# Kernel tuning notes

Hardware: AMD Instinct MI355X
Metric: run time of the kernel (lower is better)

## Reference

```python
import jax, jax.numpy as jnp
import numpy as np

DIM = 2048          # args.dim
E = 16              # n_routed_experts
TOPK = 2            # n_activated_experts
H = 1408            # moe_inter_dim (expert hidden)
N_SHARED = 2        # n_shared_experts
HS = H * N_SHARED   # shared expert hidden
B, S = 2, 2048
TEMP = 1.0          # gate_temperature


def setup_inputs() -> dict:
    key = jax.random.key(0)
    ks = jax.random.split(key, 8)
    sc = 0.02
    return {
        "x": jax.random.normal(ks[0], (B, S, DIM), dtype=jnp.float32),
        "gate_w": jax.random.normal(ks[1], (E, DIM), dtype=jnp.float32) * sc,
        "w1": jax.random.normal(ks[2], (E, H, DIM), dtype=jnp.float32) * sc,
        "w2": jax.random.normal(ks[3], (E, DIM, H), dtype=jnp.float32) * sc,
        "w3": jax.random.normal(ks[4], (E, H, DIM), dtype=jnp.float32) * sc,
        "sw1": jax.random.normal(ks[5], (HS, DIM), dtype=jnp.float32) * sc,
        "sw2": jax.random.normal(ks[6], (DIM, HS), dtype=jnp.float32) * sc,
        "sw3": jax.random.normal(ks[7], (HS, DIM), dtype=jnp.float32) * sc,
    }


def reference(x, gate_w, w1, w2, w3, sw1, sw2, sw3):
    b, s, d = x.shape
    xf = x.reshape(-1, d)  # [T, D]

    # shared expert (SwiGLU FFN)
    sh = jax.nn.silu(xf @ sw1.T) * (xf @ sw3.T)      # [T, HS]
    shared_out = sh @ sw2.T                           # [T, D]

    # gate (eval mode: no input noise)
    scores = (xf @ gate_w.T) / TEMP                   # [T, E]
    probs = jax.nn.softmax(scores, axis=-1)
    topk_vals, topk_idx = jax.lax.top_k(probs, TOPK)  # sorted desc, matches torch.topk
    topk_vals = topk_vals / (topk_vals.sum(-1, keepdims=True) + 1e-9)

    # combine weights per (token, expert); zero where expert not selected
    w = (jax.nn.one_hot(topk_idx, E, dtype=xf.dtype) * topk_vals[..., None]).sum(1)  # [T, E]

    # all-expert SwiGLU, weighted-combined (w==0 exactly zeroes unselected experts)
    h1 = jnp.einsum('td,ehd->teh', xf, w1)            # [T, E, H]
    h3 = jnp.einsum('td,ehd->teh', xf, w3)
    act = jax.nn.silu(h1) * h3 * w[:, :, None]
    y = jnp.einsum('teh,edh->td', act, w2) + shared_out

    # aux load-balancing loss
    importance = probs.mean(0)                        # [E]
    load = w.sum(0) / (w.sum() + 1e-9)                # [E]
    aux_loss = E * (importance * load).sum()

    return y.reshape(b, s, d), aux_loss
```

## Files before the change

### kernel.cpp

```cpp
#include <hip/hip_runtime.h>
#include <cstdint>

#define TOKS 4096
#define DIMD 2048
#define NE   16
#define HE   1408
#define HSH  2816
#define SLOTS 8192
#define SLOTP 8320
#define MAXT 2048

typedef unsigned short u16;
typedef __attribute__((ext_vector_type(8))) __bf16 bf16x8;
typedef __attribute__((ext_vector_type(4))) float  f32x4;

__device__ inline unsigned f2bf_pack(float a, float b) {
  unsigned ua = __builtin_bit_cast(unsigned, a);
  unsigned ub = __builtin_bit_cast(unsigned, b);
  ua = (ua + 0x7FFFu + ((ua >> 16) & 1u)) >> 16;
  ub = (ub + 0x7FFFu + ((ub >> 16) & 1u)) >> 16;
  return ua | (ub << 16);
}
__device__ inline u16 f2bf(float a) {
  unsigned ua = __builtin_bit_cast(unsigned, a);
  return (u16)((ua + 0x7FFFu + ((ua >> 16) & 1u)) >> 16);
}
__device__ inline float bf2f(u16 u) {
  return __builtin_bit_cast(float, (unsigned)u << 16);
}
__device__ inline void gload_lds16(const u16* g, u16* l) {
  __builtin_amdgcn_global_load_lds((const __attribute__((address_space(1))) void*)g,
                                   (__attribute__((address_space(3))) void*)l, 16, 0, 0);
}

__global__ __launch_bounds__(64)
void gate2_kernel(const float* __restrict__ x, const float* __restrict__ gw,
                  float* __restrict__ probs, int* __restrict__ sel0, int* __restrict__ sel1,
                  float* __restrict__ wt0, float* __restrict__ wt1,
                  u16* __restrict__ xbf)
{
  const int t = blockIdx.x;
  const int l = threadIdx.x;
  const float4* xr = (const float4*)(x + (size_t)t * DIMD);
  float4 xv[8];
#pragma unroll
  for (int j = 0; j < 8; ++j) xv[j] = xr[j * 64 + l];

  uint2* xo = (uint2*)(xbf + (size_t)t * DIMD);
#pragma unroll
  for (int j = 0; j < 8; ++j) {
    uint2 q; q.x = f2bf_pack(xv[j].x, xv[j].y); q.y = f2bf_pack(xv[j].z, xv[j].w);
    xo[j * 64 + l] = q;
  }

  float sc[16];
#pragma unroll
  for (int e = 0; e < 16; ++e) {
    const float4* g = (const float4*)(gw + (size_t)e * DIMD);
    float s = 0.f;
#pragma unroll
    for (int j = 0; j < 8; ++j) {
      float4 gv = g[j * 64 + l];
      s += xv[j].x * gv.x + xv[j].y * gv.y + xv[j].z * gv.z + xv[j].w * gv.w;
    }
#pragma unroll
    for (int o = 32; o > 0; o >>= 1) s += __shfl_down(s, o);
    sc[e] = s;
  }
  if (l == 0) {
    float mx = sc[0];
#pragma unroll
    for (int e = 1; e < 16; ++e) mx = fmaxf(mx, sc[e]);
    float pe[16]; float sum = 0.f;
#pragma unroll
    for (int e = 0; e < 16; ++e) { pe[e] = __expf(sc[e] - mx); sum += pe[e]; }
    float inv = 1.f / sum;
    int b0 = -1, b1 = -1; float v0 = -1.f, v1 = -1.f;
#pragma unroll
    for (int e = 0; e < 16; ++e) {
      float p = pe[e] * inv;
      probs[t * 16 + e] = p;
      if (p > v0) { v1 = v0; b1 = b0; v0 = p; b0 = e; }
      else if (p > v1) { v1 = p; b1 = e; }
    }
    float wsum = v0 + v1 + 1e-9f;
    sel0[t] = b0; sel1[t] = b1;
    wt0[t] = v0 / wsum; wt1[t] = v1 / wsum;
  }
}

__global__ __launch_bounds__(256)
void expert_count(const int* __restrict__ sel0, const int* __restrict__ sel1,
                  const float* __restrict__ wt0, const float* __restrict__ wt1,
                  int* __restrict__ counts, float* __restrict__ loadsum)
{
  const int e = blockIdx.x, tid = threadIdx.x;
  int c = 0; float s = 0.f;
  for (int t = tid; t < TOKS; t += 256) {
    if (sel0[t] == e) { c++; s += wt0[t]; }
    else if (sel1[t] == e) { c++; s += wt1[t]; }
  }
  __shared__ int ci[256]; __shared__ float sf[256];
  ci[tid] = c; sf[tid] = s; __syncthreads();
  for (int d = 128; d > 0; d >>= 1) {
    if (tid < d) { ci[tid] += ci[tid + d]; sf[tid] += sf[tid + d]; }
    __syncthreads();
  }
  if (tid == 0) { counts[e] = ci[0]; loadsum[e] = sf[0]; }
}

__global__ __launch_bounds__(256)
void offsets_aux(const float* __restrict__ probs, const int* __restrict__ counts,
                 const float* __restrict__ loadsum, int* __restrict__ offs,
                 int* __restrict__ te2, int* __restrict__ tn2, int* __restrict__ tm2,
                 int* __restrict__ me2,
                 int* __restrict__ te3, int* __restrict__ tn3, int* __restrict__ tm3,
                 int* __restrict__ me3,
                 float* __restrict__ out_aux)
{
  const int tid = threadIdx.x;
  float imp[16];
#pragma unroll
  for (int e = 0; e < 16; ++e) imp[e] = 0.f;
  for (int t = tid; t < TOKS; t += 256)
#pragma unroll
    for (int e = 0; e < 16; ++e) imp[e] += probs[t * 16 + e];

  __shared__ float red[256];
  __shared__ float impE[16];
  for (int e = 0; e < 16; ++e) {
    red[tid] = imp[e]; __syncthreads();
    for (int d = 128; d > 0; d >>= 1) {
      if (tid < d) red[tid] += red[tid + d];
      __syncthreads();
    }
    if (tid == 0) impE[e] = red[0];
    __syncthreads();
  }
  if (tid == 0) {
    int off = 0;
    for (int e = 0; e < 16; ++e) { offs[e] = off; off += counts[e]; }
    float tot = 0.f;
    for (int e = 0; e < 16; ++e) tot += loadsum[e];
    float aux = 0.f;
    for (int e = 0; e < 16; ++e) aux += (impE[e] / (float)TOKS) * (loadsum[e] / (tot + 1e-9f));
    *out_aux = 16.f * aux;
  }
  __syncthreads();
  if (tid < 16) {
    int e = tid;
    int mt_e = (counts[e] + 127) >> 7;
    {
      int base = 0;
      for (int ee = 0; ee < e; ++ee) base += ((counts[ee] + 127) >> 7) * 22;
      int idx = base;
      for (int n = 0; n < 22; ++n)
        for (int m = 0; m < mt_e; ++m) { te2[idx] = e; tn2[idx] = n; tm2[idx] = m << 7; ++idx; }
      if (e == 15) me2[0] = idx;
    }
    {
      int base = 0;
      for (int ee = 0; ee < e; ++ee) base += ((counts[ee] + 127) >> 7) * 16;
      int idx = base;
      for (int n = 0; n < 16; ++n)
        for (int m = 0; m < mt_e; ++m) { te3[idx] = e; tn3[idx] = n; tm3[idx] = m << 7; ++idx; }
      if (e == 15) me3[0] = idx;
    }
  }
}

__global__ __launch_bounds__(256)
void rank_scatter(const int* __restrict__ sel0, const int* __restrict__ sel1,
                  const float* __restrict__ wt0, const float* __restrict__ wt1,
                  const int* __restrict__ offs, int* __restrict__ toklist2,
                  float* __restrict__ slotwt, int* __restrict__ tokslot)
{
  const int e = blockIdx.x, tid = threadIdx.x;
  const int t0 = tid * 16;
  unsigned flags = 0; int cloc = 0;
#pragma unroll
  for (int j = 0; j < 16; ++j) {
    int t = t0 + j;
    bool f = (sel0[t] == e) || (sel1[t] == e);
    flags |= ((unsigned)f) << j;
    cloc += f;
  }
  __shared__ int psum[256];
  psum[tid] = cloc; __syncthreads();
  for (int d = 1; d < 256; d <<= 1) {
    int v = (tid >= d) ? psum[tid - d] : 0;
    __syncthreads();
    psum[tid] += v;
    __syncthreads();
  }
  int r = offs[e] + psum[tid] - cloc;
  for (int j = 0; j < 16; ++j) {
    if ((flags >> j) & 1u) {
      int t = t0 + j;
      bool first = (sel0[t] == e);
      toklist2[r] = t;
      slotwt[r] = first ? wt0[t] : wt1[t];
      tokslot[2 * t + (first ? 0 : 1)] = r;
      r++;
    }
  }
}

__global__ __launch_bounds__(256)
void cvt_f32_bf16(const float4* __restrict__ src, uint2* __restrict__ dst, int n4)
{
  int i = blockIdx.x * 256 + threadIdx.x;
  int stride = gridDim.x * 256;
  for (; i < n4; i += stride) {
    float4 v = src[i];
    uint2 p; p.x = f2bf_pack(v.x, v.y); p.y = f2bf_pack(v.z, v.w);
    dst[i] = p;
  }
}

__global__ __launch_bounds__(256)
void cvt_pair(const float4* __restrict__ src1, const float4* __restrict__ src3,
              uint2* __restrict__ dst, int rows, int k4, int dstride4, int total4)
{
  int i = blockIdx.x * 256 + threadIdx.x;
  int stride = gridDim.x * 256;
  int per_e = rows * k4;
  for (; i < total4; i += stride) {
    int e = i / per_e;
    int rem = i - e * per_e;
    int j = rem / k4;
    int c = rem - j * k4;
    size_t dbase = (size_t)e * dstride4 + (size_t)(((j >> 6) * 128 + (j & 63))) * k4 + c;
    float4 v1 = src1[i];
    uint2 p1; p1.x = f2bf_pack(v1.x, v1.y); p1.y = f2bf_pack(v1.z, v1.w);
    dst[dbase] = p1;
    float4 v3 = src3[i];
    uint2 p3; p3.x = f2bf_pack(v3.x, v3.y); p3.y = f2bf_pack(v3.z, v3.w);
    dst[dbase + (size_t)64 * k4] = p3;
  }
}

__global__ __launch_bounds__(256)
void gather2(const u16* __restrict__ xbf, const int* __restrict__ toklist2,
             u16* __restrict__ Xg)
{
  int slot = blockIdx.x * 4 + (threadIdx.x >> 6);
  int l = threadIdx.x & 63;
  int tok = toklist2[slot];
  const uint2* srcr = (const uint2*)(xbf + (size_t)tok * DIMD);
  uint2* dstr = (uint2*)(Xg + (size_t)slot * DIMD);
#pragma unroll
  for (int j = 0; j < 8; ++j) dstr[j * 64 + l] = srcr[j * 64 + l];
}

template<int MODE>
__global__ __launch_bounds__(256, 4)
void gemm128(const u16* __restrict__ A, const u16* __restrict__ Bg,
             u16* __restrict__ Obf, float* __restrict__ Of,
             const int* __restrict__ counts, const int* __restrict__ offs,
             const int* __restrict__ te, const int* __restrict__ tn,
             const int* __restrict__ tm, const int* __restrict__ meta,
             const float* __restrict__ slotwt)
{
  constexpr int KD = (MODE == 0) ? DIMD : (MODE == 1) ? HSH : (MODE == 2) ? DIMD : HE;
  constexpr int ND = (MODE == 0) ? 2 * HSH : (MODE == 1) ? DIMD : (MODE == 2) ? HSH : DIMD;
  constexpr bool FUSE = (MODE == 0 || MODE == 2);
  constexpr int NDOUT = (MODE == 0) ? HSH : (MODE == 2) ? HE : ND;

  __shared__ __align__(16) char sMemRaw[FUSE ? 36864 : 32768];
  u16* sA = (u16*)sMemRaw;
  u16* sB = sA + 128 * 64;

  const int tid  = threadIdx.x;
  const int lane = tid & 63;
  const int wave = tid >> 6;
  const int wm = wave >> 1, wn = wave & 1;

  int mbase, nbase;
  int e = 0, cnt = 0, arow0;
  const u16* B = Bg;
  if constexpr (MODE >= 2) {
    int tix = blockIdx.x;
    if (tix >= meta[0]) return;
    e = te[tix];
    cnt = counts[e];
    mbase = tm[tix];
    nbase = tn[tix] * 128;
    arow0 = offs[e] + mbase;
    B = Bg + (size_t)e * ND * KD;
  } else {
    const int nx = gridDim.x;
    int bid = blockIdx.y * nx + blockIdx.x;
    int cpx = (nx * gridDim.y) >> 3;
    int swz = (bid & 7) * cpx + (bid >> 3);
    mbase = (swz / nx) * 128;
    nbase = (swz % nx) * 128;
    arow0 = mbase;
  }

  f32x4 acc[4][4];
#pragma unroll
  for (int i = 0; i < 4; ++i)
#pragma unroll
    for (int j = 0; j < 4; ++j) acc[i][j] = (f32x4){0.f, 0.f, 0.f, 0.f};

  const int srow  = lane >> 3;
  const int sslot = (lane & 7) ^ srow;
  const int scol  = sslot * 8;

  const u16* Bbase = B + (size_t)nbase * KD;

  for (int kb = 0; kb < KD; kb += 64) {
#pragma unroll
    for (int i = 0; i < 4; ++i) {
      int c = wave * 4 + i;
      int row = c * 8 + srow;
      size_t ar;
      if constexpr (MODE >= 2) {
        int rg = arow0 + row;
        if (rg > SLOTS - 1) rg = SLOTS - 1;
        ar = (size_t)rg * KD;
      } else {
        ar = (size_t)(arow0 + row) * KD;
      }
      gload_lds16(A + ar + kb + scol, &sA[c * 512]);
      gload_lds16(Bbase + (size_t)row * KD + kb + scol, &sB[c * 512]);
    }
    __syncthreads();

#pragma unroll
    for (int ks = 0; ks < 2; ++ks) {
      bf16x8 a[4], b[4];
#pragma unroll
      for (int mi = 0; mi < 4; ++mi) {
        int r = wm * 64 + mi * 16 + (lane & 15);
        int s = (ks * 4 + (lane >> 4)) ^ (r & 7);
        a[mi] = *(const bf16x8*)((const char*)sA + r * 128 + s * 16);
      }
#pragma unroll
      for (int ni = 0; ni < 4; ++ni) {
        int r = wn * 64 + ni * 16 + (lane & 15);
        int s = (ks * 4 + (lane >> 4)) ^ (r & 7);
        b[ni] = *(const bf16x8*)((const char*)sB + r * 128 + s * 16);
      }
#pragma unroll
      for (int mi = 0; mi < 4; ++mi)
#pragma unroll
        for (int ni = 0; ni < 4; ++ni)
          acc[mi][ni] = __builtin_amdgcn_mfma_f32_16x16x32_bf16(a[mi], b[ni], acc[mi][ni], 0, 0, 0);
    }
    __syncthreads();
  }

  const int lr4 = (lane >> 4) * 4;
  const int lc  = lane & 15;

  if constexpr (FUSE) {
    float* sX = (float*)sMemRaw;
    if (wn == 1) {
#pragma unroll
      for (int mi = 0; mi < 4; ++mi)
#pragma unroll
        for (int ni = 0; ni < 4; ++ni)
#pragma unroll
          for (int r = 0; r < 4; ++r)
            sX[(wm * 64 + mi * 16 + lr4 + r) * 72 + ni * 16 + lc] = acc[mi][ni][r];
    }
    __syncthreads();
    if (wn == 0) {
#pragma unroll
      for (int mi = 0; mi < 4; ++mi) {
#pragma unroll
        for (int ni = 0; ni < 4; ++ni) {
#pragma unroll
          for (int r = 0; r < 4; ++r) {
            int lrow = wm * 64 + mi * 16 + lr4 + r;
            float h1 = acc[mi][ni][r];
            float h3 = sX[lrow * 72 + ni * 16 + lc];
            float u = (h1 / (1.f + __expf(-h1))) * h3;
            int col = (nbase >> 1) + ni * 16 + lc;
            if constexpr (MODE == 0) {
              Obf[(size_t)(mbase + lrow) * NDOUT + col] = f2bf(u);
            } else {
              int grow = mbase + lrow;
              if (grow < cnt) {
                u *= slotwt[arow0 + lrow];
                Obf[(size_t)(arow0 + lrow) * NDOUT + col] = f2bf(u);
              }
            }
          }
        }
      }
    }
  } else {
#pragma unroll
    for (int mi = 0; mi < 4; ++mi) {
#pragma unroll
      for (int ni = 0; ni < 4; ++ni) {
#pragma unroll
        for (int r = 0; r < 4; ++r) {
          int lrow = wm * 64 + mi * 16 + lr4 + r;
          int col  = nbase + wn * 64 + ni * 16 + lc;
          float v = acc[mi][ni][r];
          if constexpr (MODE == 1) {
            Of[(size_t)(mbase + lrow) * ND + col] = v;
          } else {
            int grow = mbase + lrow;
            if (grow < cnt) Obf[(size_t)(arow0 + lrow) * ND + col] = f2bf(v);
          }
        }
      }
    }
  }
}

__global__ __launch_bounds__(256)
void finalize(const u16* __restrict__ Yslot, const int* __restrict__ tokslot,
              float* __restrict__ out)
{
  int i = blockIdx.x * 256 + threadIdx.x;
  int t = i >> 8;
  int c = (i & 255) * 8;
  int s0 = tokslot[2 * t], s1 = tokslot[2 * t + 1];
  uint4 a = *(const uint4*)(Yslot + (size_t)s0 * DIMD + c);
  uint4 b = *(const uint4*)(Yslot + (size_t)s1 * DIMD + c);
  const u16* ap = (const u16*)&a;
  const u16* bp = (const u16*)&b;
  float* op = out + (size_t)t * DIMD + c;
  float4 v0 = *(float4*)op, v1 = *(float4*)(op + 4);
  float vv[8] = {v0.x, v0.y, v0.z, v0.w, v1.x, v1.y, v1.z, v1.w};
#pragma unroll
  for (int j = 0; j < 8; ++j) vv[j] += bf2f(ap[j]) + bf2f(bp[j]);
  *(float4*)op = (float4){vv[0], vv[1], vv[2], vv[3]};
  *(float4*)(op + 4) = (float4){vv[4], vv[5], vv[6], vv[7]};
}

extern "C" void kernel_launch(void* const* d_in, const int* in_sizes, int n_in,
                              void* d_out, int out_size, void* d_ws, size_t ws_size,
                              hipStream_t stream) {
  const float* x      = (const float*)d_in[0];
  const float* gate_w = (const float*)d_in[1];
  const float* w1     = (const float*)d_in[2];
  const float* w2     = (const float*)d_in[3];
  const float* w3     = (const float*)d_in[4];
  const float* sw1    = (const float*)d_in[5];
  const float* sw2    = (const float*)d_in[6];
  const float* sw3    = (const float*)d_in[7];
  float* out = (float*)d_out;

  char* ws = (char*)d_ws;
  size_t o = 0;
  int*   counts   = (int*)(ws + o);   o += 256;
  int*   offsv    = (int*)(ws + o);   o += 256;
  float* loadsum  = (float*)(ws + o); o += 256;
  int*   te2      = (int*)(ws + o);   o += MAXT * 4;
  int*   tn2      = (int*)(ws + o);   o += MAXT * 4;
  int*   tm2      = (int*)(ws + o);   o += MAXT * 4;
  int*   me2      = (int*)(ws + o);   o += 256;
  int*   te3      = (int*)(ws + o);   o += MAXT * 4;
  int*   tn3      = (int*)(ws + o);   o += MAXT * 4;
  int*   tm3      = (int*)(ws + o);   o += MAXT * 4;
  int*   me3      = (int*)(ws + o);   o += 256;
  int*   sel0     = (int*)(ws + o);   o += TOKS * 4;
  int*   sel1     = (int*)(ws + o);   o += TOKS * 4;
  float* wt0      = (float*)(ws + o); o += TOKS * 4;
  float* wt1      = (float*)(ws + o); o += TOKS * 4;
  int*   tokslot  = (int*)(ws + o);   o += TOKS * 2 * 4;
  int*   toklist2 = (int*)(ws + o);   o += SLOTS * 4;
  float* slotwt   = (float*)(ws + o); o += SLOTS * 4;
  float* probs    = (float*)(ws + o); o += TOKS * 16 * 4;

  o = 1 << 20;
  u16* xbf   = (u16*)(ws + o); o += (size_t)TOKS * DIMD * 2;
  u16* Xg    = (u16*)(ws + o); o += (size_t)SLOTP * DIMD * 2;
  u16* w13b  = (u16*)(ws + o); o += (size_t)NE * HSH * DIMD * 2;
  u16* w2b   = (u16*)(ws + o); o += (size_t)NE * DIMD * HE * 2;
  u16* sw13b = (u16*)(ws + o); o += (size_t)(2 * HSH) * DIMD * 2;
  u16* sw2b  = (u16*)(ws + o); o += (size_t)DIMD * HSH * 2;
  u16* UA    = (u16*)(ws + o); o += (size_t)SLOTP * HSH * 2;
  u16* Yslot = Xg;

  gate2_kernel<<<TOKS, 64, 0, stream>>>(x, gate_w, probs, sel0, sel1, wt0, wt1, xbf);
  expert_count<<<NE, 256, 0, stream>>>(sel0, sel1, wt0, wt1, counts, loadsum);
  offsets_aux<<<1, 256, 0, stream>>>(probs, counts, loadsum, offsv,
                                     te2, tn2, tm2, me2, te3, tn3, tm3, me3,
                                     out + (size_t)TOKS * DIMD);
  rank_scatter<<<NE, 256, 0, stream>>>(sel0, sel1, wt0, wt1, offsv, toklist2, slotwt, tokslot);

  cvt_pair<<<2048, 256, 0, stream>>>((const float4*)sw1, (const float4*)sw3, (uint2*)sw13b,
                                     HSH, DIMD / 4, 0, HSH * DIMD / 4);
  cvt_f32_bf16<<<1024, 256, 0, stream>>>((const float4*)sw2, (uint2*)sw2b, DIMD * HSH / 4);
  cvt_f32_bf16<<<4096, 256, 0, stream>>>((const float4*)w2, (uint2*)w2b, NE * DIMD * HE / 4);
  cvt_pair<<<4096, 256, 0, stream>>>((const float4*)w1, (const float4*)w3, (uint2*)w13b,
                                     HE, DIMD / 4, HSH * DIMD / 4, NE * HE * DIMD / 4);
  gather2<<<SLOTS / 4, 256, 0, stream>>>(xbf, toklist2, Xg);

  gemm128<0><<<dim3(2 * HSH / 128, TOKS / 128), 256, 0, stream>>>(
      xbf, sw13b, UA, nullptr, nullptr, nullptr, nullptr, nullptr, nullptr, nullptr, nullptr);
  gemm128<1><<<dim3(DIMD / 128, TOKS / 128), 256, 0, stream>>>(
      UA, sw2b, nullptr, out, nullptr, nullptr, nullptr, nullptr, nullptr, nullptr, nullptr);

  gemm128<2><<<dim3(22 * 80), 256, 0, stream>>>(
      Xg, w13b, UA, nullptr, counts, offsv, te2, tn2, tm2, me2, slotwt);
  gemm128<3><<<dim3(16 * 80), 256, 0, stream>>>(
      UA, w2b, Yslot, nullptr, counts, offsv, te3, tn3, tm3, me3, nullptr);
  finalize<<<TOKS * DIMD / 8 / 256, 256, 0, stream>>>(Yslot, tokslot, out);
}
```

Baseline: 765.7 us.

## Reorder grouped expert GEMM tiles into 8 interleaved spans for XCD locality

Builds the expert GEMM tile schedule so that consecutive expert/N-tile groups land on the same one of 8 interleaved block-index lanes. Round-robin block dispatch then keeps each expert's weights on one chiplet's L2, which is meant to raise cache reuse of B tiles and A rows. Unused slots are marked -1 and exit early, and the launch grows to MAXT blocks. The fused epilogue's LDS row stride also shrinks from 72 to 66 floats, which cuts shared memory but may change bank conflicts. The schedule is now built serially by a single thread, adding some latency to offsets_aux.

```diff
diff --git a/kernel.cpp b/kernel.cpp
--- a/kernel.cpp
+++ b/kernel.cpp
@@ -113,12 +113,12 @@
 void offsets_aux(const float* __restrict__ probs, const int* __restrict__ counts,
                  const float* __restrict__ loadsum, int* __restrict__ offs,
                  int* __restrict__ te2, int* __restrict__ tn2, int* __restrict__ tm2,
-                 int* __restrict__ me2,
                  int* __restrict__ te3, int* __restrict__ tn3, int* __restrict__ tm3,
-                 int* __restrict__ me3,
                  float* __restrict__ out_aux)
 {
   const int tid = threadIdx.x;
+  for (int i = tid; i < MAXT; i += 256) { te2[i] = -1; te3[i] = -1; }
+
   float imp[16];
 #pragma unroll
   for (int e = 0; e < 16; ++e) imp[e] = 0.f;
@@ -145,26 +145,42 @@
     float aux = 0.f;
     for (int e = 0; e < 16; ++e) aux += (impE[e] / (float)TOKS) * (loadsum[e] / (tot + 1e-9f));
     *out_aux = 16.f * aux;
-  }
-  __syncthreads();
-  if (tid < 16) {
-    int e = tid;
-    int mt_e = (counts[e] + 127) >> 7;
+
+    int mt[16];
+    for (int e = 0; e < 16; ++e) mt[e] = (counts[e] + 127) >> 7;
     {
-      int base = 0;
-      for (int ee = 0; ee < e; ++ee) base += ((counts[ee] + 127) >> 7) * 22;
-      int idx = base;
-      for (int n = 0; n < 22; ++n)
-        for (int m = 0; m < mt_e; ++m) { te2[idx] = e; tn2[idx] = n; tm2[idx] = m << 7; ++idx; }
-      if (e == 15) me2[0] = idx;
+      int btot = 0;
+      for (int e = 0; e < 16; ++e) btot += mt[e] * 22;
+      int target = (btot + 7) >> 3;
+      int x = 0, sp = 0;
+      for (int e = 0; e < 16; ++e) {
+        if (!mt[e]) continue;
+        for (int n = 0; n < 22; ++n) {
+          for (int m = 0; m < mt[e]; ++m) {
+            int tix = (sp + m) * 8 + x;
+            te2[tix] = e; tn2[tix] = n; tm2[tix] = m << 7;
+          }
+          sp += mt[e];
+          if (sp >= target && x < 7) { ++x; sp = 0; }
+        }
+      }
     }
     {
-      int base = 0;
-      for (int ee = 0; ee < e; ++ee) base += ((counts[ee] + 127) >> 7) * 16;
-      int idx = base;
-      for (int n = 0; n < 16; ++n)
-        for (int m = 0; m < mt_e; ++m) { te3[idx] = e; tn3[idx] = n; tm3[idx] = m << 7; ++idx; }
-      if (e == 15) me3[0] = idx;
+      int btot = 0;
+      for (int e = 0; e < 16; ++e) btot += mt[e] * 16;
+      int target = (btot + 7) >> 3;
+      int x = 0, sp = 0;
+      for (int e = 0; e < 16; ++e) {
+        if (!mt[e]) continue;
+        for (int n = 0; n < 16; ++n) {
+          for (int m = 0; m < mt[e]; ++m) {
+            int tix = (sp + m) * 8 + x;
+            te3[tix] = e; tn3[tix] = n; tm3[tix] = m << 7;
+          }
+          sp += mt[e];
+          if (sp >= target && x < 7) { ++x; sp = 0; }
+        }
+      }
     }
   }
 }
@@ -259,7 +275,7 @@
              u16* __restrict__ Obf, float* __restrict__ Of,
              const int* __restrict__ counts, const int* __restrict__ offs,
              const int* __restrict__ te, const int* __restrict__ tn,
-             const int* __restrict__ tm, const int* __restrict__ meta,
+             const int* __restrict__ tm,
              const float* __restrict__ slotwt)
 {
   constexpr int KD = (MODE == 0) ? DIMD : (MODE == 1) ? HSH : (MODE == 2) ? DIMD : HE;
@@ -267,7 +283,7 @@
   constexpr bool FUSE = (MODE == 0 || MODE == 2);
   constexpr int NDOUT = (MODE == 0) ? HSH : (MODE == 2) ? HE : ND;
 
-  __shared__ __align__(16) char sMemRaw[FUSE ? 36864 : 32768];
+  __shared__ __align__(16) char sMemRaw[FUSE ? 33792 : 32768];
   u16* sA = (u16*)sMemRaw;
   u16* sB = sA + 128 * 64;
 
@@ -281,8 +297,8 @@
   const u16* B = Bg;
   if constexpr (MODE >= 2) {
     int tix = blockIdx.x;
-    if (tix >= meta[0]) return;
     e = te[tix];
+    if (e < 0) return;
     cnt = counts[e];
     mbase = tm[tix];
     nbase = tn[tix] * 128;
@@ -364,7 +380,7 @@
         for (int ni = 0; ni < 4; ++ni)
 #pragma unroll
           for (int r = 0; r < 4; ++r)
-            sX[(wm * 64 + mi * 16 + lr4 + r) * 72 + ni * 16 + lc] = acc[mi][ni][r];
+            sX[(wm * 64 + mi * 16 + lr4 + r) * 66 + ni * 16 + lc] = acc[mi][ni][r];
     }
     __syncthreads();
     if (wn == 0) {
@@ -376,7 +392,7 @@
           for (int r = 0; r < 4; ++r) {
             int lrow = wm * 64 + mi * 16 + lr4 + r;
             float h1 = acc[mi][ni][r];
-            float h3 = sX[lrow * 72 + ni * 16 + lc];
+            float h3 = sX[lrow * 66 + ni * 16 + lc];
             float u = (h1 / (1.f + __expf(-h1))) * h3;
             int col = (nbase >> 1) + ni * 16 + lc;
             if constexpr (MODE == 0) {
@@ -456,11 +472,9 @@
   int*   te2      = (int*)(ws + o);   o += MAXT * 4;
   int*   tn2      = (int*)(ws + o);   o += MAXT * 4;
   int*   tm2      = (int*)(ws + o);   o += MAXT * 4;
-  int*   me2      = (int*)(ws + o);   o += 256;
   int*   te3      = (int*)(ws + o);   o += MAXT * 4;
   int*   tn3      = (int*)(ws + o);   o += MAXT * 4;
   int*   tm3      = (int*)(ws + o);   o += MAXT * 4;
-  int*   me3      = (int*)(ws + o);   o += 256;
   int*   sel0     = (int*)(ws + o);   o += TOKS * 4;
   int*   sel1     = (int*)(ws + o);   o += TOKS * 4;
   float* wt0      = (float*)(ws + o); o += TOKS * 4;
@@ -483,7 +497,7 @@
   gate2_kernel<<<TOKS, 64, 0, stream>>>(x, gate_w, probs, sel0, sel1, wt0, wt1, xbf);
   expert_count<<<NE, 256, 0, stream>>>(sel0, sel1, wt0, wt1, counts, loadsum);
   offsets_aux<<<1, 256, 0, stream>>>(probs, counts, loadsum, offsv,
-                                     te2, tn2, tm2, me2, te3, tn3, tm3, me3,
+                                     te2, tn2, tm2, te3, tn3, tm3,
                                      out + (size_t)TOKS * DIMD);
   rank_scatter<<<NE, 256, 0, stream>>>(sel0, sel1, wt0, wt1, offsv, toklist2, slotwt, tokslot);
 
@@ -496,13 +510,13 @@
   gather2<<<SLOTS / 4, 256, 0, stream>>>(xbf, toklist2, Xg);
 
   gemm128<0><<<dim3(2 * HSH / 128, TOKS / 128), 256, 0, stream>>>(
-      xbf, sw13b, UA, nullptr, nullptr, nullptr, nullptr, nullptr, nullptr, nullptr, nullptr);
+      xbf, sw13b, UA, nullptr, nullptr, nullptr, nullptr, nullptr, nullptr, nullptr);
   gemm128<1><<<dim3(DIMD / 128, TOKS / 128), 256, 0, stream>>>(
-      UA, sw2b, nullptr, out, nullptr, nullptr, nullptr, nullptr, nullptr, nullptr, nullptr);
-
-  gemm128<2><<<dim3(22 * 80), 256, 0, stream>>>(
-      Xg, w13b, UA, nullptr, counts, offsv, te2, tn2, tm2, me2, slotwt);
-  gemm128<3><<<dim3(16 * 80), 256, 0, stream>>>(
-      UA, w2b, Yslot, nullptr, counts, offsv, te3, tn3, tm3, me3, nullptr);
+      UA, sw2b, nullptr, out, nullptr, nullptr, nullptr, nullptr, nullptr, nullptr);
+
+  gemm128<2><<<dim3(MAXT), 256, 0, stream>>>(
+      Xg, w13b, UA, nullptr, counts, offsv, te2, tn2, tm2, slotwt);
+  gemm128<3><<<dim3(MAXT), 256, 0, stream>>>(
+      UA, w2b, Yslot, nullptr, counts, offsv, te3, tn3, tm3, nullptr);
   finalize<<<TOKS * DIMD / 8 / 256, 256, 0, stream>>>(Yslot, tokslot, out);
 }
```

Measured after the change: 875.3 us. +14.3%, slower.
